# Kernel optimization log

Hardware: AMD Instinct MI355X
Metric: run time of the kernel (lower is better)

The kernel has to match this reference:

```python
import jax, jax.numpy as jnp
import numpy as np

D_EMB = 1024
N_HEADS = 16


def setup_inputs() -> dict:
    key = jax.random.key(0)
    k_x, k_wq, k_bq, k_wp, k_bp = jax.random.split(key, 5)
    B, N, D = 8, 1024, D_EMB
    x = jax.random.normal(k_x, (B, N, D), dtype=jnp.float32)
    s = 1.0 / np.sqrt(D)
    w_qkv = jax.random.normal(k_wq, (D, 3 * D), dtype=jnp.float32) * s
    b_qkv = jax.random.normal(k_bq, (3 * D,), dtype=jnp.float32) * 0.01
    w_proj = jax.random.normal(k_wp, (D, D), dtype=jnp.float32) * s
    b_proj = jax.random.normal(k_bp, (D,), dtype=jnp.float32) * 0.01
    return {"x": x, "w_qkv": w_qkv, "b_qkv": b_qkv, "w_proj": w_proj, "b_proj": b_proj}


def reference(x, w_qkv, b_qkv, w_proj, b_proj):
    B, N, D = x.shape
    H = N_HEADS
    d = D // H
    qkv = x @ w_qkv + b_qkv                      # [B, N, 3D]
    # einops '(h d qkv)': qkv index is the innermost factor of the last dim
    qkv = qkv.reshape(B, N, H, d, 3)
    q = qkv[..., 0]                              # [B, N, H, d]
    k = qkv[..., 1]
    v = qkv[..., 2]
    score = jnp.einsum('bqhd,bkhd->bhqk', q, k)  # [B, H, N, N]
    # module scales AFTER softmax, by sqrt(d_emb) (not sqrt(d_head))
    att = jax.nn.softmax(score, axis=-1) / jnp.sqrt(jnp.float32(D))
    out = jnp.einsum('bhqk,bkhd->bqhd', att, v).reshape(B, N, D)
    return out @ w_proj + b_proj
```

## Files before the change

### kernel.cpp

```cpp
#include <hip/hip_runtime.h>
#include <hip/hip_bf16.h>
#include <stdint.h>

typedef __hip_bfloat16 bf16;
typedef __attribute__((ext_vector_type(8))) short short8;
typedef __attribute__((ext_vector_type(4))) float f32x4;
typedef __attribute__((ext_vector_type(16))) float f32x16;

#define MFMA16(a, b, c) __builtin_amdgcn_mfma_f32_16x16x32_bf16(a, b, c, 0, 0, 0)
#define MFMA32(a, b, c) __builtin_amdgcn_mfma_f32_32x32x16_bf16(a, b, c, 0, 0, 0)

#define BATCH 8
#define SEQ   1024
#define DEMB  1024
#define NH    16
#define DH    64
#define MTOT  (BATCH * SEQ)

__device__ __forceinline__ float rdf(const void* p, size_t idx, int isf) {
  if (isf) return ((const float*)p)[idx];
  return __bfloat162float(((const bf16*)p)[idx]);
}

__device__ __forceinline__ unsigned int pk2(float a, float b) {
  unsigned short ua = __bfloat16_as_ushort(__float2bfloat16(a));
  unsigned short ub = __bfloat16_as_ushort(__float2bfloat16(b));
  return (unsigned int)ua | ((unsigned int)ub << 16);
}

union U4S8 { uint4 u; short8 s; };

__device__ __forceinline__ void gload16(const bf16* g, bf16* l) {
  __builtin_amdgcn_global_load_lds(
      (const __attribute__((address_space(1))) void*)g,
      (__attribute__((address_space(3))) void*)l, 16, 0, 0);
}

__global__ void detect_dtype(const unsigned int* __restrict__ xw, int* __restrict__ flag) {
  int lane = threadIdx.x;
  float v = __uint_as_float(xw[lane]);
  bool isf32 = (fabsf(v) < 1e20f);
  unsigned long long m = __ballot(isf32);
  if (lane == 0) flag[0] = (__popcll(m) >= 32) ? 1 : 0;
}

__global__ __launch_bounds__(256) void convert_x(
    const void* __restrict__ xin, bf16* __restrict__ xc, const int* __restrict__ flag) {
  const int isf = flag[0];
  size_t i = ((size_t)blockIdx.x * 256 + threadIdx.x) * 8;
  if (isf) {
    const float* xf = (const float*)xin;
    float4 a = *(const float4*)&xf[i];
    float4 b = *(const float4*)&xf[i + 4];
    bf16 o[8];
    o[0] = __float2bfloat16(a.x); o[1] = __float2bfloat16(a.y);
    o[2] = __float2bfloat16(a.z); o[3] = __float2bfloat16(a.w);
    o[4] = __float2bfloat16(b.x); o[5] = __float2bfloat16(b.y);
    o[6] = __float2bfloat16(b.z); o[7] = __float2bfloat16(b.w);
    *(int4*)&xc[i] = *(const int4*)&o[0];
  } else {
    *(int4*)&xc[i] = *(const int4*)&((const bf16*)xin)[i];
  }
}

__global__ __launch_bounds__(256) void permute_wqkv(
    const void* __restrict__ w, const void* __restrict__ b,
    bf16* __restrict__ wt, float* __restrict__ bqp, const int* __restrict__ flag) {
  __shared__ __attribute__((aligned(16))) bf16 ls[192][66];
  const int isf = flag[0];
  const int t = threadIdx.x;
  const int k0 = blockIdx.x * 64;
  const int h = blockIdx.y;
#pragma unroll
  for (int i = 0; i < 48; ++i) {
    int e = t + i * 256;
    int k = e / 192, c = e % 192;
    ls[c][k] = __float2bfloat16(rdf(w, (size_t)(k0 + k) * 3072 + h * 192 + c, isf));
  }
  if (blockIdx.x == 0 && t < 192) {
    int dd = t / 3, j = t % 3;
    bqp[j * 1024 + h * 64 + dd] = rdf(b, h * 192 + t, isf);
  }
  __syncthreads();
#pragma unroll
  for (int i = 0; i < 48; ++i) {
    int e = t + i * 256;
    int c = e / 64, k = e & 63;
    int dd = c / 3, j = c % 3;
    wt[(size_t)(j * 1024 + h * 64 + dd) * 1024 + k0 + k] = ls[c][k];
  }
}

__global__ __launch_bounds__(256) void transpose_wp(
    const void* __restrict__ w, bf16* __restrict__ wt, const int* __restrict__ flag) {
  __shared__ __attribute__((aligned(16))) bf16 ls[64][66];
  const int isf = flag[0];
  const int t = threadIdx.x;
  const int r0 = blockIdx.y * 64;
  const int c0 = blockIdx.x * 64;
#pragma unroll
  for (int i = 0; i < 16; ++i) {
    int e = t + i * 256;
    int r = e >> 6, c = e & 63;
    ls[c][r] = __float2bfloat16(rdf(w, (size_t)(r0 + r) * 1024 + c0 + c, isf));
  }
  __syncthreads();
#pragma unroll
  for (int i = 0; i < 16; ++i) {
    int e = t + i * 256;
    int c = e >> 6, r = e & 63;
    wt[(size_t)(c0 + c) * 1024 + r0 + r] = ls[c][r];
  }
}

__device__ __forceinline__ void gemm256_core(
    const bf16* __restrict__ A, const bf16* __restrict__ Bt,
    int m0, int n0, bf16* lds, f32x4 acc[8][4]) {
  const int t = threadIdx.x;
  const int lane = t & 63, w = t >> 6;
  const int l15 = lane & 15, quad = lane >> 4;
  const int wm = w >> 2, wn = w & 3;

  const int sr = lane >> 2;
  const int sc = (lane & 3) * 8;
  const bf16* gA = A + (size_t)(m0 + w * 16 + sr) * 1024 + sc;
  const bf16* gB = Bt + (size_t)(n0 + w * 16 + sr) * 1024 + sc;

#pragma unroll
  for (int tt = 0; tt < 3; ++tt) {
    bf16* sb = lds + tt * 16384;
    gload16(gA + tt * 32, sb + w * 512);
    gload16(gA + tt * 32 + 131072, sb + 4096 + w * 512);
    gload16(gB + tt * 32, sb + 8192 + w * 512);
    gload16(gB + tt * 32 + 131072, sb + 12288 + w * 512);
  }
  asm volatile("s_waitcnt vmcnt(8)" ::: "memory");
  __builtin_amdgcn_s_barrier();

#pragma unroll 4
  for (int tau = 0; tau < 32; ++tau) {
    const int slot = tau & 3;
    const int pf = (tau + 3) & 3;
    const int kpf = ((tau + 3) & 31) * 32;
    const bf16* ls = lds + slot * 16384;
    bf16* sb = lds + pf * 16384;

    short8 afr[4], bfr[4];
    const bf16* pa0 = ls + (wm * 128 + l15) * 32 + quad * 8;
#pragma unroll
    for (int i = 0; i < 4; ++i) afr[i] = *(const short8*)(pa0 + i * 512);
    const bf16* pb0 = ls + 8192 + (wn * 64 + l15) * 32 + quad * 8;
#pragma unroll
    for (int j = 0; j < 4; ++j) bfr[j] = *(const short8*)(pb0 + j * 512);
    gload16(gA + kpf, sb + w * 512);
    gload16(gA + kpf + 131072, sb + 4096 + w * 512);
    asm volatile("" ::: "memory");
    __builtin_amdgcn_s_barrier();
    asm volatile("s_waitcnt lgkmcnt(0)" ::: "memory");
    __builtin_amdgcn_s_setprio(1);
#pragma unroll
    for (int i = 0; i < 4; ++i)
#pragma unroll
      for (int j = 0; j < 4; ++j)
        acc[i][j] = MFMA16(afr[i], bfr[j], acc[i][j]);
    __builtin_amdgcn_s_setprio(0);
    asm volatile("" ::: "memory");
    __builtin_amdgcn_s_barrier();

    const bf16* pa1 = pa0 + 64 * 32;
#pragma unroll
    for (int i = 0; i < 4; ++i) afr[i] = *(const short8*)(pa1 + i * 512);
    gload16(gB + kpf, sb + 8192 + w * 512);
    gload16(gB + kpf + 131072, sb + 12288 + w * 512);
    asm volatile("" ::: "memory");
    __builtin_amdgcn_s_barrier();
    asm volatile("s_waitcnt lgkmcnt(0)" ::: "memory");
    __builtin_amdgcn_s_setprio(1);
#pragma unroll
    for (int i = 0; i < 4; ++i)
#pragma unroll
      for (int j = 0; j < 4; ++j)
        acc[4 + i][j] = MFMA16(afr[i], bfr[j], acc[4 + i][j]);
    __builtin_amdgcn_s_setprio(0);
    asm volatile("s_waitcnt vmcnt(8)" ::: "memory");
    asm volatile("" ::: "memory");
    __builtin_amdgcn_s_barrier();
  }
  asm volatile("s_waitcnt vmcnt(0)" ::: "memory");
}

__global__ __launch_bounds__(512, 2) void gemm256_qkv(
    const bf16* __restrict__ A, const bf16* __restrict__ Bt,
    const float* __restrict__ bias,
    bf16* __restrict__ qb, bf16* __restrict__ kb, bf16* __restrict__ vb) {
  extern __shared__ bf16 smem[];
  const int t = threadIdx.x;
  const int lane = t & 63;
  const int l15 = lane & 15, quad = lane >> 4;
  const int w = t >> 6, wm = w >> 2, wn = w & 3;
  const int bid = blockIdx.x;
  const int swz = (bid & 7) * 48 + (bid >> 3);
  const int m0 = (swz / 12) * 256;
  const int n0 = (swz % 12) * 256;

  f32x4 acc[8][4];
  const f32x4 zero = {0.f, 0.f, 0.f, 0.f};
#pragma unroll
  for (int i = 0; i < 8; ++i)
#pragma unroll
    for (int j = 0; j < 4; ++j) acc[i][j] = zero;

  gemm256_core(A, Bt, m0, n0, smem, acc);

  const int jj = n0 >> 10;
  const int hh = ((n0 + wn * 64) & 1023) >> 6;
#pragma unroll
  for (int fi = 0; fi < 8; ++fi) {
    int m = m0 + wm * 128 + fi * 16 + quad * 4;
    int bb = m >> 10, nidx = m & 1023;
    size_t bhq = (size_t)(bb * NH + hh);
#pragma unroll
    for (int fj = 0; fj < 4; ++fj) {
      int dd = fj * 16 + l15;
      float bv = bias[n0 + wn * 64 + dd];
      if (jj == 2) {
        unsigned int lo = pk2(acc[fi][fj][0] + bv, acc[fi][fj][1] + bv);
        unsigned int hi = pk2(acc[fi][fj][2] + bv, acc[fi][fj][3] + bv);
        *(uint2*)&vb[(bhq * 64 + dd) * 1024 + nidx] = make_uint2(lo, hi);
      } else {
        bf16* dst = (jj == 0) ? qb : kb;
#pragma unroll
        for (int r = 0; r < 4; ++r)
          dst[(bhq * 1024 + (size_t)(nidx + r)) * 64 + dd] =
              __float2bfloat16(acc[fi][fj][r] + bv);
      }
    }
  }
}

__global__ __launch_bounds__(256, 4) void attn(
    const bf16* __restrict__ qb, const bf16* __restrict__ kb,
    const bf16* __restrict__ vb, bf16* __restrict__ ob) {
  const int t = threadIdx.x, lane = t & 63, w = t >> 6;
  const int q5 = lane & 31, half = lane >> 5;
  const int bh = blockIdx.y;
  const int bat = bh >> 4, h = bh & 15;
  const int q0 = blockIdx.x * 128;
  const int qrow = q0 + w * 32 + q5;

  __shared__ __attribute__((aligned(16))) bf16 lsK[64][72];
  __shared__ __attribute__((aligned(16))) bf16 lsV[64][72];

  const bf16* qp = qb + (size_t)bh * (1024 * 64);
  const bf16* kp = kb + (size_t)bh * (1024 * 64);
  const bf16* vp = vb + (size_t)bh * (64 * 1024);

  short8 bq[4];
#pragma unroll
  for (int kk = 0; kk < 4; ++kk)
    bq[kk] = *(const short8*)&qp[(size_t)qrow * 64 + kk * 16 + half * 8];

  float m_run = -1e30f, l_run = 0.f;
  f32x16 po[2];
#pragma unroll
  for (int r = 0; r < 16; ++r) { po[0][r] = 0.f; po[1][r] = 0.f; }

  const int sr = t >> 3;
  const int sc = (t & 7) * 8;

  for (int kt = 0; kt < 1024; kt += 64) {
    int4 g0 = *(const int4*)&kp[(size_t)(kt + sr) * 64 + sc];
    int4 g1 = *(const int4*)&kp[(size_t)(kt + 32 + sr) * 64 + sc];
    int4 g2 = *(const int4*)&vp[(size_t)sr * 1024 + kt + sc];
    int4 g3 = *(const int4*)&vp[(size_t)(32 + sr) * 1024 + kt + sc];
    __syncthreads();
    *(int4*)&lsK[sr][sc] = g0;
    *(int4*)&lsK[32 + sr][sc] = g1;
    *(int4*)&lsV[sr][sc] = g2;
    *(int4*)&lsV[32 + sr][sc] = g3;
    __syncthreads();

    f32x16 st[2];
#pragma unroll
    for (int r = 0; r < 16; ++r) { st[0][r] = 0.f; st[1][r] = 0.f; }
#pragma unroll
    for (int kk = 0; kk < 4; ++kk) {
#pragma unroll
      for (int tj = 0; tj < 2; ++tj) {
        short8 ak = *(const short8*)&lsK[tj * 32 + q5][kk * 16 + half * 8];
        st[tj] = MFMA32(ak, bq[kk], st[tj]);
      }
    }

    float smax = st[0][0];
#pragma unroll
    for (int r = 1; r < 16; ++r) smax = fmaxf(smax, st[0][r]);
#pragma unroll
    for (int r = 0; r < 16; ++r) smax = fmaxf(smax, st[1][r]);
    smax = fmaxf(smax, __shfl_xor(smax, 32));
    float mnew = fmaxf(m_run, smax);
    float alpha = __expf(m_run - mnew);
    m_run = mnew;
    float lsum = 0.f;
#pragma unroll
    for (int tj = 0; tj < 2; ++tj)
#pragma unroll
      for (int r = 0; r < 16; ++r) {
        float p = __expf(st[tj][r] - mnew);
        st[tj][r] = p;
        lsum += p;
      }
    lsum += __shfl_xor(lsum, 32);
    l_run = l_run * alpha + lsum;
#pragma unroll
    for (int r = 0; r < 16; ++r) { po[0][r] *= alpha; po[1][r] *= alpha; }

#pragma unroll
    for (int kk2 = 0; kk2 < 4; ++kk2) {
      const int nbA = 2 * kk2, nbB = 2 * kk2 + 1;
      unsigned int a0 = pk2(st[nbA >> 2][4 * (nbA & 3) + 0], st[nbA >> 2][4 * (nbA & 3) + 1]);
      unsigned int a1 = pk2(st[nbA >> 2][4 * (nbA & 3) + 2], st[nbA >> 2][4 * (nbA & 3) + 3]);
      unsigned int b0 = pk2(st[nbB >> 2][4 * (nbB & 3) + 0], st[nbB >> 2][4 * (nbB & 3) + 1]);
      unsigned int b1 = pk2(st[nbB >> 2][4 * (nbB & 3) + 2], st[nbB >> 2][4 * (nbB & 3) + 3]);
      unsigned int s0 = half ? a0 : b0;
      unsigned int s1 = half ? a1 : b1;
      unsigned int r0 = (unsigned int)__shfl_xor((int)s0, 32);
      unsigned int r1 = (unsigned int)__shfl_xor((int)s1, 32);
      U4S8 fr;
      fr.u.x = half ? r0 : a0;
      fr.u.y = half ? r1 : a1;
      fr.u.z = half ? b0 : r0;
      fr.u.w = half ? b1 : r1;
#pragma unroll
      for (int ti = 0; ti < 2; ++ti) {
        short8 av = *(const short8*)&lsV[ti * 32 + q5][kk2 * 16 + half * 8];
        po[ti] = MFMA32(av, fr.s, po[ti]);
      }
    }
  }

  float inv = 1.0f / (l_run * 32.0f);
  bf16* op = ob + ((size_t)(bat * 1024 + qrow)) * 1024 + h * 64;
#pragma unroll
  for (int ti = 0; ti < 2; ++ti)
#pragma unroll
    for (int g = 0; g < 4; ++g) {
      unsigned int lo = pk2(po[ti][4 * g + 0] * inv, po[ti][4 * g + 1] * inv);
      unsigned int hi = pk2(po[ti][4 * g + 2] * inv, po[ti][4 * g + 3] * inv);
      uint2 u = make_uint2(lo, hi);
      *(uint2*)&op[ti * 32 + g * 8 + half * 4] = u;
    }
}

__global__ __launch_bounds__(512, 2) void gemm256_proj(
    const bf16* __restrict__ A, const bf16* __restrict__ Bt,
    const void* __restrict__ bias, float* __restrict__ out,
    const int* __restrict__ flag) {
  extern __shared__ bf16 smem[];
  const int t = threadIdx.x;
  const int lane = t & 63;
  const int l15 = lane & 15, quad = lane >> 4;
  const int w = t >> 6, wm = w >> 2, wn = w & 3;
  const int bid = blockIdx.x;
  const int swz = (bid & 7) * 16 + (bid >> 3);
  const int m0 = (swz >> 2) * 256;
  const int n0 = (swz & 3) * 256;

  f32x4 acc[8][4];
  const f32x4 zero = {0.f, 0.f, 0.f, 0.f};
#pragma unroll
  for (int i = 0; i < 8; ++i)
#pragma unroll
    for (int j = 0; j < 4; ++j) acc[i][j] = zero;

  gemm256_core(A, Bt, m0, n0, smem, acc);

  const int isf = flag[0];
#pragma unroll
  for (int fj = 0; fj < 4; ++fj) {
    int c = n0 + wn * 64 + fj * 16 + l15;
    float bv = rdf(bias, c, isf);
#pragma unroll
    for (int fi = 0; fi < 8; ++fi) {
      int m = m0 + wm * 128 + fi * 16 + quad * 4;
#pragma unroll
      for (int r = 0; r < 4; ++r)
        out[(size_t)(m + r) * 1024 + c] = acc[fi][fj][r] + bv;
    }
  }
}

extern "C" void kernel_launch(void* const* d_in, const int* in_sizes, int n_in,
                              void* d_out, int out_size, void* d_ws, size_t ws_size,
                              hipStream_t stream) {
  const void* x      = d_in[0];
  const void* w_qkv  = d_in[1];
  const void* b_qkv  = d_in[2];
  const void* w_proj = d_in[3];
  const void* b_proj = d_in[4];
  float* out = (float*)d_out;

  char* ws = (char*)d_ws;
  bf16*  wt_qkv = (bf16*)(ws);
  float* bqp    = (float*)(ws + 6291456);
  bf16*  wtp    = (bf16*)(ws + 6303744);
  bf16*  xc     = (bf16*)(ws + 8400896);
  bf16*  q_buf  = (bf16*)(ws + 25178112);
  bf16*  k_buf  = (bf16*)(ws + 41955328);
  bf16*  v_buf  = (bf16*)(ws + 58732544);
  int*   flag   = (int*)(ws + 75509760);
  bf16*  att    = xc;

  static bool lds_attr_done = false;
  if (!lds_attr_done) {
    (void)hipFuncSetAttribute(reinterpret_cast<const void*>(gemm256_qkv),
                              hipFuncAttributeMaxDynamicSharedMemorySize, 131072);
    (void)hipFuncSetAttribute(reinterpret_cast<const void*>(gemm256_proj),
                              hipFuncAttributeMaxDynamicSharedMemorySize, 131072);
    lds_attr_done = true;
  }

  detect_dtype<<<1, 64, 0, stream>>>((const unsigned int*)x, flag);
  convert_x<<<4096, 256, 0, stream>>>(x, xc, flag);
  permute_wqkv<<<dim3(16, 16), 256, 0, stream>>>(w_qkv, b_qkv, wt_qkv, bqp, flag);
  transpose_wp<<<dim3(16, 16), 256, 0, stream>>>(w_proj, wtp, flag);
  gemm256_qkv<<<dim3(384), 512, 131072, stream>>>(xc, wt_qkv, bqp, q_buf, k_buf, v_buf);
  attn<<<dim3(8, 128), 256, 0, stream>>>(q_buf, k_buf, v_buf, att);
  gemm256_proj<<<dim3(128), 512, 131072, stream>>>(att, wtp, b_proj, out, flag);
}
```

Before: 289.0 us.

## Swizzle LDS layout in GEMM core and use 128x256 tiles for projection

Adds an XOR swizzle to the global-to-LDS load columns and the matching LDS fragment reads in the GEMM cores, to cut LDS bank conflicts. The output-projection GEMM moves to a new 128x256 tile core with 3-buffer-sized slots and 256 blocks instead of 128, so more of the CUs have work. The smaller M tile gives less reuse of B per block and relies on the swizzle being consistent between the async loads and the reads.

```diff
diff --git a/kernel.cpp b/kernel.cpp
--- a/kernel.cpp
+++ b/kernel.cpp
@@ -113,6 +113,7 @@
   }
 }
 
+
 __device__ __forceinline__ void gemm256_core(
     const bf16* __restrict__ A, const bf16* __restrict__ Bt,
     int m0, int n0, bf16* lds, f32x4 acc[8][4]) {
@@ -122,9 +123,9 @@
   const int wm = w >> 2, wn = w & 3;
 
   const int sr = lane >> 2;
-  const int sc = (lane & 3) * 8;
-  const bf16* gA = A + (size_t)(m0 + w * 16 + sr) * 1024 + sc;
-  const bf16* gB = Bt + (size_t)(n0 + w * 16 + sr) * 1024 + sc;
+  const int scs = (((lane & 3) ^ ((lane >> 3) & 3))) * 8;
+  const bf16* gA = A + (size_t)(m0 + w * 16 + sr) * 1024 + scs;
+  const bf16* gB = Bt + (size_t)(n0 + w * 16 + sr) * 1024 + scs;
 
 #pragma unroll
   for (int tt = 0; tt < 3; ++tt) {
@@ -137,19 +138,22 @@
   asm volatile("s_waitcnt vmcnt(8)" ::: "memory");
   __builtin_amdgcn_s_barrier();
 
+  const int swz8 = ((quad ^ (l15 >> 1)) & 3) * 8;
+  const bf16* paBase = lds + (wm * 128 + l15) * 32 + swz8;
+  const bf16* pbBase = lds + 8192 + (wn * 64 + l15) * 32 + swz8;
+
 #pragma unroll 4
   for (int tau = 0; tau < 32; ++tau) {
     const int slot = tau & 3;
     const int pf = (tau + 3) & 3;
     const int kpf = ((tau + 3) & 31) * 32;
-    const bf16* ls = lds + slot * 16384;
+    const bf16* pa0 = paBase + slot * 16384;
+    const bf16* pb0 = pbBase + slot * 16384;
     bf16* sb = lds + pf * 16384;
 
     short8 afr[4], bfr[4];
-    const bf16* pa0 = ls + (wm * 128 + l15) * 32 + quad * 8;
 #pragma unroll
     for (int i = 0; i < 4; ++i) afr[i] = *(const short8*)(pa0 + i * 512);
-    const bf16* pb0 = ls + 8192 + (wn * 64 + l15) * 32 + quad * 8;
 #pragma unroll
     for (int j = 0; j < 4; ++j) bfr[j] = *(const short8*)(pb0 + j * 512);
     gload16(gA + kpf, sb + w * 512);
@@ -183,6 +187,65 @@
         acc[4 + i][j] = MFMA16(afr[i], bfr[j], acc[4 + i][j]);
     __builtin_amdgcn_s_setprio(0);
     asm volatile("s_waitcnt vmcnt(8)" ::: "memory");
+    asm volatile("" ::: "memory");
+    __builtin_amdgcn_s_barrier();
+  }
+  asm volatile("s_waitcnt vmcnt(0)" ::: "memory");
+}
+
+__device__ __forceinline__ void gemm128x256_core(
+    const bf16* __restrict__ A, const bf16* __restrict__ Bt,
+    int m0, int n0, bf16* lds, f32x4 acc[4][4]) {
+  const int t = threadIdx.x;
+  const int lane = t & 63, w = t >> 6;
+  const int l15 = lane & 15, quad = lane >> 4;
+  const int wm = w >> 2, wn = w & 3;
+  const int sr = lane >> 2;
+  const int scs = (((lane & 3) ^ ((lane >> 3) & 3))) * 8;
+  const bf16* gA = A + (size_t)(m0 + w * 16 + sr) * 1024 + scs;
+  const bf16* gB = Bt + (size_t)(n0 + w * 16 + sr) * 1024 + scs;
+
+#pragma unroll
+  for (int tt = 0; tt < 3; ++tt) {
+    bf16* sb = lds + tt * 12288;
+    gload16(gA + tt * 32, sb + w * 512);
+    gload16(gB + tt * 32, sb + 4096 + w * 512);
+    gload16(gB + tt * 32 + 131072, sb + 8192 + w * 512);
+  }
+  asm volatile("s_waitcnt vmcnt(6)" ::: "memory");
+  __builtin_amdgcn_s_barrier();
+
+  const int swz8 = ((quad ^ (l15 >> 1)) & 3) * 8;
+  const bf16* paBase = lds + (wm * 64 + l15) * 32 + swz8;
+  const bf16* pbBase = lds + 4096 + (wn * 64 + l15) * 32 + swz8;
+
+#pragma unroll 4
+  for (int tau = 0; tau < 32; ++tau) {
+    const int slot = tau & 3;
+    const int pf = (tau + 3) & 3;
+    const int kpf = ((tau + 3) & 31) * 32;
+    const bf16* pa = paBase + slot * 12288;
+    const bf16* pb = pbBase + slot * 12288;
+    bf16* sb = lds + pf * 12288;
+    short8 afr[4], bfr[4];
+#pragma unroll
+    for (int i = 0; i < 4; ++i) afr[i] = *(const short8*)(pa + i * 512);
+#pragma unroll
+    for (int j = 0; j < 4; ++j) bfr[j] = *(const short8*)(pb + j * 512);
+    gload16(gA + kpf, sb + w * 512);
+    gload16(gB + kpf, sb + 4096 + w * 512);
+    gload16(gB + kpf + 131072, sb + 8192 + w * 512);
+    asm volatile("" ::: "memory");
+    __builtin_amdgcn_s_barrier();
+    asm volatile("s_waitcnt lgkmcnt(0)" ::: "memory");
+    __builtin_amdgcn_s_setprio(1);
+#pragma unroll
+    for (int i = 0; i < 4; ++i)
+#pragma unroll
+      for (int j = 0; j < 4; ++j)
+        acc[i][j] = MFMA16(afr[i], bfr[j], acc[i][j]);
+    __builtin_amdgcn_s_setprio(0);
+    asm volatile("s_waitcnt vmcnt(6)" ::: "memory");
     asm volatile("" ::: "memory");
     __builtin_amdgcn_s_barrier();
   }
@@ -362,18 +425,18 @@
   const int l15 = lane & 15, quad = lane >> 4;
   const int w = t >> 6, wm = w >> 2, wn = w & 3;
   const int bid = blockIdx.x;
-  const int swz = (bid & 7) * 16 + (bid >> 3);
-  const int m0 = (swz >> 2) * 256;
+  const int swz = (bid & 7) * 32 + (bid >> 3);
+  const int m0 = (swz >> 2) * 128;
   const int n0 = (swz & 3) * 256;
 
-  f32x4 acc[8][4];
+  f32x4 acc[4][4];
   const f32x4 zero = {0.f, 0.f, 0.f, 0.f};
 #pragma unroll
-  for (int i = 0; i < 8; ++i)
+  for (int i = 0; i < 4; ++i)
 #pragma unroll
     for (int j = 0; j < 4; ++j) acc[i][j] = zero;
 
-  gemm256_core(A, Bt, m0, n0, smem, acc);
+  gemm128x256_core(A, Bt, m0, n0, smem, acc);
 
   const int isf = flag[0];
 #pragma unroll
@@ -381,8 +444,8 @@
     int c = n0 + wn * 64 + fj * 16 + l15;
     float bv = rdf(bias, c, isf);
 #pragma unroll
-    for (int fi = 0; fi < 8; ++fi) {
-      int m = m0 + wm * 128 + fi * 16 + quad * 4;
+    for (int fi = 0; fi < 4; ++fi) {
+      int m = m0 + wm * 64 + fi * 16 + quad * 4;
 #pragma unroll
       for (int r = 0; r < 4; ++r)
         out[(size_t)(m + r) * 1024 + c] = acc[fi][fj][r] + bv;
@@ -426,5 +489,5 @@
   transpose_wp<<<dim3(16, 16), 256, 0, stream>>>(w_proj, wtp, flag);
   gemm256_qkv<<<dim3(384), 512, 131072, stream>>>(xc, wt_qkv, bqp, q_buf, k_buf, v_buf);
   attn<<<dim3(8, 128), 256, 0, stream>>>(q_buf, k_buf, v_buf, att);
-  gemm256_proj<<<dim3(128), 512, 131072, stream>>>(att, wtp, b_proj, out, flag);
-}
+  gemm256_proj<<<dim3(256), 512, 98304, stream>>>(att, wtp, b_proj, out, flag);
+}
```

Measured after the change: 270.2 us. 1.07x faster.

## Replace LDS-staged GEMM pipeline with direct global-to-register fragment loads

Applied to the files above, without the earlier changes.

The QKV and projection GEMMs drop the 4-stage LDS ring buffer (global_load_lds plus barriers). Each wave now loads its MFMA fragments straight from global memory into registers, double-buffered. The projection GEMM also moves to 128x256 tiles on a 256-block grid. This removes barrier and LDS traffic overhead and the dynamic shared memory, but it loses operand sharing between waves, so global and cache load traffic grows and accesses are less coalesced.

```diff
diff --git a/kernel.cpp b/kernel.cpp
--- a/kernel.cpp
+++ b/kernel.cpp
@@ -29,12 +29,6 @@
 }
 
 union U4S8 { uint4 u; short8 s; };
-
-__device__ __forceinline__ void gload16(const bf16* g, bf16* l) {
-  __builtin_amdgcn_global_load_lds(
-      (const __attribute__((address_space(1))) void*)g,
-      (__attribute__((address_space(3))) void*)l, 16, 0, 0);
-}
 
 __global__ void detect_dtype(const unsigned int* __restrict__ xw, int* __restrict__ flag) {
   int lane = threadIdx.x;
@@ -113,87 +107,51 @@
   }
 }
 
-__device__ __forceinline__ void gemm256_core(
+template <int MF>
+__device__ __forceinline__ void gemm_direct_core(
     const bf16* __restrict__ A, const bf16* __restrict__ Bt,
-    int m0, int n0, bf16* lds, f32x4 acc[8][4]) {
-  const int t = threadIdx.x;
-  const int lane = t & 63, w = t >> 6;
+    int m0, int n0, f32x4 acc[MF][4]) {
+  const int t = threadIdx.x;
+  const int lane = t & 63;
   const int l15 = lane & 15, quad = lane >> 4;
-  const int wm = w >> 2, wn = w & 3;
-
-  const int sr = lane >> 2;
-  const int sc = (lane & 3) * 8;
-  const bf16* gA = A + (size_t)(m0 + w * 16 + sr) * 1024 + sc;
-  const bf16* gB = Bt + (size_t)(n0 + w * 16 + sr) * 1024 + sc;
-
-#pragma unroll
-  for (int tt = 0; tt < 3; ++tt) {
-    bf16* sb = lds + tt * 16384;
-    gload16(gA + tt * 32, sb + w * 512);
-    gload16(gA + tt * 32 + 131072, sb + 4096 + w * 512);
-    gload16(gB + tt * 32, sb + 8192 + w * 512);
-    gload16(gB + tt * 32 + 131072, sb + 12288 + w * 512);
-  }
-  asm volatile("s_waitcnt vmcnt(8)" ::: "memory");
-  __builtin_amdgcn_s_barrier();
-
-#pragma unroll 4
-  for (int tau = 0; tau < 32; ++tau) {
-    const int slot = tau & 3;
-    const int pf = (tau + 3) & 3;
-    const int kpf = ((tau + 3) & 31) * 32;
-    const bf16* ls = lds + slot * 16384;
-    bf16* sb = lds + pf * 16384;
-
-    short8 afr[4], bfr[4];
-    const bf16* pa0 = ls + (wm * 128 + l15) * 32 + quad * 8;
-#pragma unroll
-    for (int i = 0; i < 4; ++i) afr[i] = *(const short8*)(pa0 + i * 512);
-    const bf16* pb0 = ls + 8192 + (wn * 64 + l15) * 32 + quad * 8;
-#pragma unroll
-    for (int j = 0; j < 4; ++j) bfr[j] = *(const short8*)(pb0 + j * 512);
-    gload16(gA + kpf, sb + w * 512);
-    gload16(gA + kpf + 131072, sb + 4096 + w * 512);
-    asm volatile("" ::: "memory");
-    __builtin_amdgcn_s_barrier();
-    asm volatile("s_waitcnt lgkmcnt(0)" ::: "memory");
-    __builtin_amdgcn_s_setprio(1);
-#pragma unroll
-    for (int i = 0; i < 4; ++i)
-#pragma unroll
-      for (int j = 0; j < 4; ++j)
-        acc[i][j] = MFMA16(afr[i], bfr[j], acc[i][j]);
-    __builtin_amdgcn_s_setprio(0);
-    asm volatile("" ::: "memory");
-    __builtin_amdgcn_s_barrier();
-
-    const bf16* pa1 = pa0 + 64 * 32;
-#pragma unroll
-    for (int i = 0; i < 4; ++i) afr[i] = *(const short8*)(pa1 + i * 512);
-    gload16(gB + kpf, sb + 8192 + w * 512);
-    gload16(gB + kpf + 131072, sb + 12288 + w * 512);
-    asm volatile("" ::: "memory");
-    __builtin_amdgcn_s_barrier();
-    asm volatile("s_waitcnt lgkmcnt(0)" ::: "memory");
-    __builtin_amdgcn_s_setprio(1);
-#pragma unroll
-    for (int i = 0; i < 4; ++i)
-#pragma unroll
-      for (int j = 0; j < 4; ++j)
-        acc[4 + i][j] = MFMA16(afr[i], bfr[j], acc[4 + i][j]);
-    __builtin_amdgcn_s_setprio(0);
-    asm volatile("s_waitcnt vmcnt(8)" ::: "memory");
-    asm volatile("" ::: "memory");
-    __builtin_amdgcn_s_barrier();
-  }
-  asm volatile("s_waitcnt vmcnt(0)" ::: "memory");
+  const int w = t >> 6, wm = w >> 2, wn = w & 3;
+
+  const bf16* pa = A + (size_t)(m0 + wm * (MF * 16) + l15) * 1024 + quad * 8;
+  const bf16* pb = Bt + (size_t)(n0 + wn * 64 + l15) * 1024 + quad * 8;
+
+  short8 fa[2][MF], fb[2][4];
+#pragma unroll
+  for (int i = 0; i < MF; ++i) fa[0][i] = *(const short8*)(pa + (size_t)i * 16 * 1024);
+#pragma unroll
+  for (int j = 0; j < 4; ++j) fb[0][j] = *(const short8*)(pb + (size_t)j * 16 * 1024);
+
+  for (int kt = 0; kt < 1024; kt += 64) {
+#pragma unroll
+    for (int p = 0; p < 2; ++p) {
+      const int knext = kt + (p + 1) * 32;
+      if (knext < 1024) {
+#pragma unroll
+        for (int i = 0; i < MF; ++i)
+          fa[p ^ 1][i] = *(const short8*)(pa + knext + (size_t)i * 16 * 1024);
+#pragma unroll
+        for (int j = 0; j < 4; ++j)
+          fb[p ^ 1][j] = *(const short8*)(pb + knext + (size_t)j * 16 * 1024);
+      }
+      __builtin_amdgcn_s_setprio(1);
+#pragma unroll
+      for (int i = 0; i < MF; ++i)
+#pragma unroll
+        for (int j = 0; j < 4; ++j)
+          acc[i][j] = MFMA16(fa[p][i], fb[p][j], acc[i][j]);
+      __builtin_amdgcn_s_setprio(0);
+    }
+  }
 }
 
 __global__ __launch_bounds__(512, 2) void gemm256_qkv(
     const bf16* __restrict__ A, const bf16* __restrict__ Bt,
     const float* __restrict__ bias,
     bf16* __restrict__ qb, bf16* __restrict__ kb, bf16* __restrict__ vb) {
-  extern __shared__ bf16 smem[];
   const int t = threadIdx.x;
   const int lane = t & 63;
   const int l15 = lane & 15, quad = lane >> 4;
@@ -210,7 +168,7 @@
 #pragma unroll
     for (int j = 0; j < 4; ++j) acc[i][j] = zero;
 
-  gemm256_core(A, Bt, m0, n0, smem, acc);
+  gemm_direct_core<8>(A, Bt, m0, n0, acc);
 
   const int jj = n0 >> 10;
   const int hh = ((n0 + wn * 64) & 1023) >> 6;
@@ -356,24 +314,23 @@
     const bf16* __restrict__ A, const bf16* __restrict__ Bt,
     const void* __restrict__ bias, float* __restrict__ out,
     const int* __restrict__ flag) {
-  extern __shared__ bf16 smem[];
   const int t = threadIdx.x;
   const int lane = t & 63;
   const int l15 = lane & 15, quad = lane >> 4;
   const int w = t >> 6, wm = w >> 2, wn = w & 3;
   const int bid = blockIdx.x;
-  const int swz = (bid & 7) * 16 + (bid >> 3);
-  const int m0 = (swz >> 2) * 256;
+  const int swz = (bid & 7) * 32 + (bid >> 3);
+  const int m0 = (swz >> 2) * 128;
   const int n0 = (swz & 3) * 256;
 
-  f32x4 acc[8][4];
+  f32x4 acc[4][4];
   const f32x4 zero = {0.f, 0.f, 0.f, 0.f};
 #pragma unroll
-  for (int i = 0; i < 8; ++i)
+  for (int i = 0; i < 4; ++i)
 #pragma unroll
     for (int j = 0; j < 4; ++j) acc[i][j] = zero;
 
-  gemm256_core(A, Bt, m0, n0, smem, acc);
+  gemm_direct_core<4>(A, Bt, m0, n0, acc);
 
   const int isf = flag[0];
 #pragma unroll
@@ -381,8 +338,8 @@
     int c = n0 + wn * 64 + fj * 16 + l15;
     float bv = rdf(bias, c, isf);
 #pragma unroll
-    for (int fi = 0; fi < 8; ++fi) {
-      int m = m0 + wm * 128 + fi * 16 + quad * 4;
+    for (int fi = 0; fi < 4; ++fi) {
+      int m = m0 + wm * 64 + fi * 16 + quad * 4;
 #pragma unroll
       for (int r = 0; r < 4; ++r)
         out[(size_t)(m + r) * 1024 + c] = acc[fi][fj][r] + bv;
@@ -411,20 +368,11 @@
   int*   flag   = (int*)(ws + 75509760);
   bf16*  att    = xc;
 
-  static bool lds_attr_done = false;
-  if (!lds_attr_done) {
-    (void)hipFuncSetAttribute(reinterpret_cast<const void*>(gemm256_qkv),
-                              hipFuncAttributeMaxDynamicSharedMemorySize, 131072);
-    (void)hipFuncSetAttribute(reinterpret_cast<const void*>(gemm256_proj),
-                              hipFuncAttributeMaxDynamicSharedMemorySize, 131072);
-    lds_attr_done = true;
-  }
-
   detect_dtype<<<1, 64, 0, stream>>>((const unsigned int*)x, flag);
   convert_x<<<4096, 256, 0, stream>>>(x, xc, flag);
   permute_wqkv<<<dim3(16, 16), 256, 0, stream>>>(w_qkv, b_qkv, wt_qkv, bqp, flag);
   transpose_wp<<<dim3(16, 16), 256, 0, stream>>>(w_proj, wtp, flag);
-  gemm256_qkv<<<dim3(384), 512, 131072, stream>>>(xc, wt_qkv, bqp, q_buf, k_buf, v_buf);
+  gemm256_qkv<<<dim3(384), 512, 0, stream>>>(xc, wt_qkv, bqp, q_buf, k_buf, v_buf);
   attn<<<dim3(8, 128), 256, 0, stream>>>(q_buf, k_buf, v_buf, att);
-  gemm256_proj<<<dim3(128), 512, 131072, stream>>>(att, wtp, b_proj, out, flag);
-}
+  gemm256_proj<<<dim3(256), 512, 0, stream>>>(att, wtp, b_proj, out, flag);
+}
```

Result: slower. 427.7 us (+48.0%).
